# Performance work log

Measured on AMD Instinct MI355X. Metric: run time of the kernel, lower is better.

## Reference

```python
import jax, jax.numpy as jnp
import numpy as np

# FlowNetC correlation config: kernel_size=1, so no kernel-window averaging;
# pad_size == max_displacement -> output spatial size == input spatial size.
B, C, H, W = 8, 256, 48, 64
MAX_DISP = 20   # max_displacement
STRIDE2 = 2     # displacement stride
PAD = 20        # pad_size
GRID_RAD = MAX_DISP // STRIDE2            # 10
GRID_W = 2 * GRID_RAD + 1                 # 21 -> 441 displacement channels


def setup_inputs() -> dict:
    key = jax.random.key(0)
    k1, k2 = jax.random.split(key)
    return {
        "input1": jax.random.normal(k1, (B, C, H, W), dtype=jnp.float32),
        "input2": jax.random.normal(k2, (B, C, H, W), dtype=jnp.float32),
    }


def _correlation(input1, input2):
    b, c, h, w = input1.shape
    p2 = jnp.pad(input2, ((0, 0), (0, 0), (PAD, PAD), (PAD, PAD)))
    # Displacement start offsets into the padded map. dy-major ordering matches
    # the CUDA kernel: top_channel = dy_idx * GRID_W + dx_idx.
    d = np.arange(-GRID_RAD, GRID_RAD + 1) * STRIDE2 + PAD  # [21]
    offs = np.stack(np.meshgrid(d, d, indexing="ij"), axis=-1).reshape(-1, 2)
    offs = jnp.asarray(offs, dtype=jnp.int32)  # [441, 2] (dy, dx)
    sumelems = jnp.float32(c)  # kernel_size^2 * C with kernel_size=1

    def step(carry, o):
        shifted = jax.lax.dynamic_slice(p2, (0, 0, o[0], o[1]), (b, c, h, w))
        # mean over channels of elementwise product -> [B, H, W]
        return carry, jnp.sum(input1 * shifted, axis=1) / sumelems

    _, ys = jax.lax.scan(step, 0, offs)          # [441, B, H, W]
    return jnp.transpose(ys, (1, 0, 2, 3))       # [B, 441, H, W]


def reference(input1, input2):
    return _correlation(input1, input2)
```

## Files before the change

kernel.cpp:

```cpp
#include <hip/hip_runtime.h>

typedef __bf16 bf16x8 __attribute__((ext_vector_type(8)));
typedef float f32x4 __attribute__((ext_vector_type(4)));
typedef float f32x16 __attribute__((ext_vector_type(16)));

#define CC 256
#define HH 48
#define WW 64
#define HW (HH * WW)
#define NB 8
#define GW 21

__global__ __launch_bounds__(256) void prep_kernel(const float* __restrict__ in1,
                                                   const float* __restrict__ in2,
                                                   unsigned short* __restrict__ o1,
                                                   unsigned short* __restrict__ o2)
{
    __shared__ float lds[CC * 33];
    int blk  = blockIdx.x;
    int sel  = (blk >= 768);
    int blk2 = sel ? blk - 768 : blk;
    int b  = blk2 & 7;
    int st = blk2 >> 3;
    int s0 = st * 32;
    const float* src = sel ? in2 : in1;
    unsigned short* dst = sel ? o2 : o1;
    float scale = sel ? 1.0f : (1.0f / 256.0f);

    int t = threadIdx.x;
    int sidx  = t & 31;
    int cbase = t >> 5;
    const float* sb = src + (size_t)b * CC * HW + s0;
    #pragma unroll
    for (int p = 0; p < 32; ++p) {
        int c = cbase + p * 8;
        lds[c * 33 + sidx] = sb[(size_t)c * HW + sidx] * scale;
    }
    __syncthreads();

    int y  = s0 >> 6;
    int xb = s0 & 63;
    int s  = t & 31;
    int c8 = t >> 5;
    unsigned short* db = dst + (size_t)(b * HH + y) * 32 * 64 * 8;
    #pragma unroll
    for (int it = 0; it < 4; ++it) {
        int cblk = it * 8 + c8;
        unsigned dw[4];
        #pragma unroll
        for (int d = 0; d < 4; ++d) {
            unsigned u0 = __builtin_bit_cast(unsigned, lds[(cblk * 8 + 2 * d) * 33 + s]);
            u0 += 0x7fffu + ((u0 >> 16) & 1u);
            unsigned u1 = __builtin_bit_cast(unsigned, lds[(cblk * 8 + 2 * d + 1) * 33 + s]);
            u1 += 0x7fffu + ((u1 >> 16) & 1u);
            dw[d] = (u0 >> 16) | (u1 & 0xffff0000u);
        }
        *(uint4*)(db + ((size_t)cblk * 64 + xb + s) * 8) =
            make_uint4(dw[0], dw[1], dw[2], dw[3]);
    }
}

__global__ __launch_bounds__(256, 4) void corr_kernel(const unsigned short* __restrict__ in1F,
                                                      const unsigned short* __restrict__ in2F,
                                                      float* __restrict__ out)
{
    __shared__ unsigned char smem[36864];
    unsigned short* Bl = (unsigned short*)smem;

    int blk  = blockIdx.x;
    int b    = blk & 7;
    int t2   = blk >> 3;
    int ysrc = t2 / 6 - 20;
    int jg   = t2 - (t2 / 6) * 6;
    int tid  = threadIdx.x;
    int w    = tid >> 6;
    int lane = tid & 63;

    int j  = 6 * w + jg;
    int yo = ysrc - 2 * (j - 10);
    bool jvalid = (j <= 20) && (yo >= 0) && (yo < HH);

    float* orow = jvalid
        ? out + (((size_t)(b * 441 + j * GW)) * HH + yo) * WW
        : out;

    if (ysrc < 0 || ysrc >= HH) {
        if (jvalid) {
            #pragma unroll
            for (int jx = 0; jx < GW; ++jx)
                __builtin_nontemporal_store(0.0f, orow + (size_t)jx * HW + lane);
        }
        return;
    }

    int l31 = lane & 31;
    int q2  = lane >> 5;

    const unsigned short* arow = jvalid
        ? in1F + (((size_t)(b * HH + yo) * 32 + q2) * 64 + l31) * 8
        : in1F;

    bf16x8 Ab[4][2], Bb[2][2];
    if (jvalid) {
        #pragma unroll
        for (int p = 0; p < 3; ++p)
            #pragma unroll
            for (int mt = 0; mt < 2; ++mt)
                Ab[p][mt] = *(const bf16x8*)(arow + (size_t)p * 1024 + mt * 256);
    }

    {
        const unsigned short* bsrc = in2F + (size_t)(b * HH + ysrc) * (32 * 64 * 8);
        #pragma unroll
        for (int it = 0; it < 8; ++it) {
            size_t off = ((size_t)it * 256 + tid) * 8;
            *(uint4*)(Bl + off) = *(const uint4*)(bsrc + off);
        }
    }
    __syncthreads();

    f32x16 acc[2][2];
    if (jvalid) {
        const unsigned short* brow = Bl + ((size_t)q2 * 64 + l31) * 8;

        #pragma unroll
        for (int mt = 0; mt < 2; ++mt)
            #pragma unroll
            for (int nt = 0; nt < 2; ++nt)
                acc[mt][nt] = (f32x16)(0.0f);

        #pragma unroll
        for (int nt = 0; nt < 2; ++nt)
            Bb[0][nt] = *(const bf16x8*)(brow + nt * 256);

        #pragma unroll
        for (int kk = 0; kk < 16; ++kk) {
            if (kk < 13) {
                #pragma unroll
                for (int mt = 0; mt < 2; ++mt)
                    Ab[(kk + 3) & 3][mt] =
                        *(const bf16x8*)(arow + (size_t)(kk + 3) * 1024 + mt * 256);
            }
            if (kk < 15) {
                #pragma unroll
                for (int nt = 0; nt < 2; ++nt)
                    Bb[(kk + 1) & 1][nt] =
                        *(const bf16x8*)(brow + (size_t)(kk + 1) * 1024 + nt * 256);
            }
            #pragma unroll
            for (int mt = 0; mt < 2; ++mt)
                #pragma unroll
                for (int nt = 0; nt < 2; ++nt)
                    acc[mt][nt] = __builtin_amdgcn_mfma_f32_32x32x16_bf16(
                        Ab[kk & 3][mt], Bb[kk & 1][nt], acc[mt][nt], 0, 0, 0);
        }
    }

    __syncthreads();

    if (!jvalid) return;

    float* dtw = (float*)smem + w * 2304;
    #pragma unroll
    for (int h = 0; h < 2; ++h) {
        #pragma unroll
        for (int nt = 0; nt < 2; ++nt) {
            #pragma unroll
            for (int rq = 0; rq < 4; ++rq) {
                f32x4 v = { acc[h][nt][4 * rq], acc[h][nt][4 * rq + 1],
                            acc[h][nt][4 * rq + 2], acc[h][nt][4 * rq + 3] };
                *(f32x4*)(dtw + (nt * 32 + l31) * 36 + rq * 8 + q2 * 4) = v;
            }
        }
        int x = h * 32 + l31;
        #pragma unroll
        for (int jj = 0; jj < 11; ++jj) {
            int jx = 2 * jj + q2;
            if (jx >= GW) continue;
            int colx = x + 2 * (jx - 10);
            float v = (colx >= 0 && colx < WW) ? dtw[colx * 36 + l31] : 0.0f;
            __builtin_nontemporal_store(v, orow + (size_t)jx * HW + x);
        }
    }
}

extern "C" void kernel_launch(void* const* d_in, const int* in_sizes, int n_in,
                              void* d_out, int out_size, void* d_ws, size_t ws_size,
                              hipStream_t stream)
{
    (void)in_sizes; (void)n_in; (void)out_size; (void)ws_size;
    const float* in1 = (const float*)d_in[0];
    const float* in2 = (const float*)d_in[1];
    float* out = (float*)d_out;

    unsigned short* in1F = (unsigned short*)d_ws;
    unsigned short* in2F = in1F + (size_t)NB * HW * CC;

    prep_kernel<<<dim3(1536), dim3(256), 0, stream>>>(in1, in2, in1F, in2F);
    corr_kernel<<<dim3(NB * 88 * 6), dim3(256), 0, stream>>>(in1F, in2F, out);
}
```

Before: 117.9 us.

## Split x by parity to drop wasted cross-parity MFMA tiles in correlation

The prep kernel now stores bf16 feature columns reordered by x parity, with even x first and odd x second. Because the horizontal displacement stride is 2, only same-parity pixel pairs are needed. The correlation kernel therefore issues two 32x32 MFMA tiles (even-even, odd-odd) instead of four, halving matrix work and accumulator registers. The epilogue gathers results using the parity layout, which adds more indexing logic to the output path.

```diff
diff --git a/kernel.cpp b/kernel.cpp
--- a/kernel.cpp
+++ b/kernel.cpp
@@ -43,6 +43,8 @@
     int s  = t & 31;
     int c8 = t >> 5;
     unsigned short* db = dst + (size_t)(b * HH + y) * 32 * 64 * 8;
+    int x = xb + s;
+    int xoff = (x & 1) * 32 + (x >> 1);
     #pragma unroll
     for (int it = 0; it < 4; ++it) {
         int cblk = it * 8 + c8;
@@ -55,7 +57,7 @@
             u1 += 0x7fffu + ((u1 >> 16) & 1u);
             dw[d] = (u0 >> 16) | (u1 & 0xffff0000u);
         }
-        *(uint4*)(db + ((size_t)cblk * 64 + xb + s) * 8) =
+        *(uint4*)(db + ((size_t)cblk * 64 + xoff) * 8) =
             make_uint4(dw[0], dw[1], dw[2], dw[3]);
     }
 }
@@ -97,16 +99,16 @@
     int q2  = lane >> 5;
 
     const unsigned short* arow = jvalid
-        ? in1F + (((size_t)(b * HH + yo) * 32 + q2) * 64 + l31) * 8
+        ? in1F + ((size_t)(b * HH + yo) * 32 + q2) * 512 + (size_t)l31 * 8
         : in1F;
 
     bf16x8 Ab[4][2], Bb[2][2];
     if (jvalid) {
         #pragma unroll
-        for (int p = 0; p < 3; ++p)
+        for (int kr = 0; kr < 3; ++kr)
             #pragma unroll
-            for (int mt = 0; mt < 2; ++mt)
-                Ab[p][mt] = *(const bf16x8*)(arow + (size_t)p * 1024 + mt * 256);
+            for (int p = 0; p < 2; ++p)
+                Ab[kr][p] = *(const bf16x8*)(arow + (size_t)kr * 1024 + p * 256);
     }
 
     {
@@ -119,40 +121,35 @@
     }
     __syncthreads();
 
-    f32x16 acc[2][2];
+    f32x16 acc[2];
     if (jvalid) {
-        const unsigned short* brow = Bl + ((size_t)q2 * 64 + l31) * 8;
+        const unsigned short* brow = Bl + (size_t)q2 * 512 + (size_t)l31 * 8;
+
+        acc[0] = (f32x16)(0.0f);
+        acc[1] = (f32x16)(0.0f);
 
         #pragma unroll
-        for (int mt = 0; mt < 2; ++mt)
-            #pragma unroll
-            for (int nt = 0; nt < 2; ++nt)
-                acc[mt][nt] = (f32x16)(0.0f);
-
-        #pragma unroll
-        for (int nt = 0; nt < 2; ++nt)
-            Bb[0][nt] = *(const bf16x8*)(brow + nt * 256);
+        for (int p = 0; p < 2; ++p)
+            Bb[0][p] = *(const bf16x8*)(brow + p * 256);
 
         #pragma unroll
         for (int kk = 0; kk < 16; ++kk) {
             if (kk < 13) {
                 #pragma unroll
-                for (int mt = 0; mt < 2; ++mt)
-                    Ab[(kk + 3) & 3][mt] =
-                        *(const bf16x8*)(arow + (size_t)(kk + 3) * 1024 + mt * 256);
+                for (int p = 0; p < 2; ++p)
+                    Ab[(kk + 3) & 3][p] =
+                        *(const bf16x8*)(arow + (size_t)(kk + 3) * 1024 + p * 256);
             }
             if (kk < 15) {
                 #pragma unroll
-                for (int nt = 0; nt < 2; ++nt)
-                    Bb[(kk + 1) & 1][nt] =
-                        *(const bf16x8*)(brow + (size_t)(kk + 1) * 1024 + nt * 256);
+                for (int p = 0; p < 2; ++p)
+                    Bb[(kk + 1) & 1][p] =
+                        *(const bf16x8*)(brow + (size_t)(kk + 1) * 1024 + p * 256);
             }
             #pragma unroll
-            for (int mt = 0; mt < 2; ++mt)
-                #pragma unroll
-                for (int nt = 0; nt < 2; ++nt)
-                    acc[mt][nt] = __builtin_amdgcn_mfma_f32_32x32x16_bf16(
-                        Ab[kk & 3][mt], Bb[kk & 1][nt], acc[mt][nt], 0, 0, 0);
+            for (int p = 0; p < 2; ++p)
+                acc[p] = __builtin_amdgcn_mfma_f32_32x32x16_bf16(
+                    Ab[kk & 3][p], Bb[kk & 1][p], acc[p], 0, 0, 0);
         }
     }
 
@@ -162,25 +159,22 @@
 
     float* dtw = (float*)smem + w * 2304;
     #pragma unroll
-    for (int h = 0; h < 2; ++h) {
+    for (int p = 0; p < 2; ++p) {
         #pragma unroll
-        for (int nt = 0; nt < 2; ++nt) {
-            #pragma unroll
-            for (int rq = 0; rq < 4; ++rq) {
-                f32x4 v = { acc[h][nt][4 * rq], acc[h][nt][4 * rq + 1],
-                            acc[h][nt][4 * rq + 2], acc[h][nt][4 * rq + 3] };
-                *(f32x4*)(dtw + (nt * 32 + l31) * 36 + rq * 8 + q2 * 4) = v;
-            }
+        for (int rq = 0; rq < 4; ++rq) {
+            f32x4 v = { acc[p][4 * rq], acc[p][4 * rq + 1],
+                        acc[p][4 * rq + 2], acc[p][4 * rq + 3] };
+            *(f32x4*)(dtw + (size_t)(p * 32 + l31) * 36 + rq * 8 + q2 * 4) = v;
         }
-        int x = h * 32 + l31;
-        #pragma unroll
-        for (int jj = 0; jj < 11; ++jj) {
-            int jx = 2 * jj + q2;
-            if (jx >= GW) continue;
-            int colx = x + 2 * (jx - 10);
-            float v = (colx >= 0 && colx < WW) ? dtw[colx * 36 + l31] : 0.0f;
-            __builtin_nontemporal_store(v, orow + (size_t)jx * HW + x);
-        }
+    }
+
+    int xe = lane >> 1;
+    int pp = lane & 1;
+    #pragma unroll
+    for (int jx = 0; jx < GW; ++jx) {
+        int ce = xe + jx - 10;
+        float v = (ce >= 0 && ce < 32) ? dtw[(size_t)(pp * 32 + ce) * 36 + xe] : 0.0f;
+        __builtin_nontemporal_store(v, orow + (size_t)jx * HW + lane);
     }
 }
 
```

After: 116.3 us. Within noise of the previous version (-1.3%).
